# Performance work log

Measured on AMD Instinct MI355X. Metric: run time of the kernel, lower is better.

## Reference

```python
import jax, jax.numpy as jnp
import numpy as np

TOP_K = 2  # matches init_kwargs top_k


def setup_inputs() -> dict:
    key = jax.random.key(0)
    ks = jax.random.split(key, 7)
    d_model, d_ff, E = 512, 2048, 8
    B, S = 2, 2048
    std = 0.02
    return {
        "x": jax.random.normal(ks[0], (B, S, d_model), dtype=jnp.float32),
        "Wr": jax.random.normal(ks[1], (E, d_model), dtype=jnp.float32) * std,
        "br": jnp.zeros((E,), dtype=jnp.float32),
        "W1": jax.random.normal(ks[2], (E, d_model, d_ff), dtype=jnp.float32) * (1.0 / np.sqrt(d_model)),
        "b1": jnp.zeros((E, d_ff), dtype=jnp.float32),
        "W2": jax.random.normal(ks[3], (E, d_ff, d_model), dtype=jnp.float32) * (1.0 / np.sqrt(d_ff)),
        "b2": jnp.zeros((E, d_model), dtype=jnp.float32),
    }


def _moe_forward(x, Wr, br, W1, b1, W2, b2):
    leading = x.shape[:-1]
    d = x.shape[-1]
    E = Wr.shape[0]
    xf = x.reshape(-1, d)                                   # [N, d]
    N = xf.shape[0]

    # --- token router (linear head) ---
    logits = xf @ Wr.T + br                                  # [N, E]
    routing = jax.nn.softmax(logits, axis=-1)                # [N, E]
    sel_w, sel_idx = jax.lax.top_k(routing, TOP_K)           # [N, K]
    sel_w = sel_w / jnp.sum(sel_w, axis=-1, keepdims=True)   # renormalize top-k

    # combine weights as dense [N, E] (zero for unselected experts)
    combine = jnp.zeros((N, E), dtype=xf.dtype).at[
        jnp.arange(N)[:, None], sel_idx
    ].add(sel_w)                                             # [N, E]

    # --- expert FFNs (dense all-expert compute, masked combine) ---
    h = jax.nn.gelu(jnp.einsum("nd,edf->enf", xf, W1) + b1[:, None, :])  # [E, N, ff]
    y = jnp.einsum("enf,efd->end", h, W2) + b2[:, None, :]               # [E, N, d]

    out = jnp.einsum("ne,end->nd", combine, y)               # [N, d]
    return out.reshape(*leading, d)


def reference(x, Wr, br, W1, b1, W2, b2):
    return _moe_forward(x, Wr, br, W1, b1, W2, b2)
```

## Files before the change

kernel.cpp:

```cpp
#include <hip/hip_runtime.h>
#include <hip/hip_bf16.h>
#include <cstdint>

typedef unsigned short u16;
typedef __bf16 bf16_t;
typedef __bf16 bf16x8 __attribute__((ext_vector_type(8)));
typedef float f32x4 __attribute__((ext_vector_type(4)));

#define DM   512
#define DFF  2048
#define NEXP 8

__device__ __forceinline__ u16 f2bf(float f) {
  bf16_t b = (bf16_t)f;
  return __builtin_bit_cast(u16, b);
}
__device__ __forceinline__ uint32_t pack_bf2(float lo, float hi) {
  return (uint32_t)f2bf(lo) | ((uint32_t)f2bf(hi) << 16);
}
__device__ __forceinline__ float gelu_tanh(float x) {
  float x3 = x * x * x;
  float z = 0.7978845608028654f * (x + 0.044715f * x3);
  float az = fabsf(z);
  float e = __expf(2.0f * az);
  float t = 1.0f - 2.0f / (e + 1.0f);
  t = copysignf(t, z);
  return 0.5f * x * (1.0f + t);
}
__device__ __forceinline__ void async16(const u16* g, u16* l) {
  __builtin_amdgcn_global_load_lds((const __attribute__((address_space(1))) void*)g,
                                   (__attribute__((address_space(3))) void*)l, 16, 0, 0);
}

__global__ void k_transpose_cvt(const float* __restrict__ src, u16* __restrict__ dst,
                                int R, int C) {
  __shared__ u16 tile[64][65];
  int e = blockIdx.y;
  int tilesC = C >> 6;
  int bR = (blockIdx.x / tilesC) << 6;
  int bC = (blockIdx.x % tilesC) << 6;
  const float* s = src + (size_t)e * R * C;
  u16* d = dst + (size_t)e * R * C;
  int lr = threadIdx.x >> 6;
  int lc = threadIdx.x & 63;
#pragma unroll
  for (int i = 0; i < 16; ++i) {
    int r = (i << 2) + lr;
    tile[r][lc] = f2bf(s[(size_t)(bR + r) * C + bC + lc]);
  }
  __syncthreads();
#pragma unroll
  for (int i = 0; i < 16; ++i) {
    int c = (i << 2) + lr;
    d[(size_t)(bC + c) * R + bR + lc] = tile[lc][c];
  }
}

__global__ void k_router(const float* __restrict__ x, const float* __restrict__ Wr,
                         const float* __restrict__ br, int* __restrict__ sel_idx,
                         float* __restrict__ sel_w, int Ntok) {
  int wid = threadIdx.x >> 6;
  int lane = threadIdx.x & 63;
  int tok = (blockIdx.x << 2) + wid;
  if (tok >= Ntok) return;
  const float4* xr = (const float4*)(x + (size_t)tok * DM);
  float4 x0 = xr[lane * 2], x1 = xr[lane * 2 + 1];
  float logit[NEXP];
#pragma unroll
  for (int e = 0; e < NEXP; ++e) {
    const float4* wr = (const float4*)(Wr + e * DM);
    float4 w0 = wr[lane * 2], w1 = wr[lane * 2 + 1];
    float p = x0.x * w0.x + x0.y * w0.y + x0.z * w0.z + x0.w * w0.w
            + x1.x * w1.x + x1.y * w1.y + x1.z * w1.z + x1.w * w1.w;
#pragma unroll
    for (int off = 32; off; off >>= 1) p += __shfl_xor(p, off, 64);
    logit[e] = p + br[e];
  }
  if (lane == 0) {
    float mx = logit[0];
#pragma unroll
    for (int e = 1; e < NEXP; ++e) mx = fmaxf(mx, logit[e]);
    float pr[NEXP];
#pragma unroll
    for (int e = 0; e < NEXP; ++e) pr[e] = __expf(logit[e] - mx);
    int i0 = 0;
#pragma unroll
    for (int e = 1; e < NEXP; ++e) if (pr[e] > pr[i0]) i0 = e;
    int i1 = -1;
#pragma unroll
    for (int e = 0; e < NEXP; ++e) {
      if (e == i0) continue;
      if (i1 < 0 || pr[e] > pr[i1]) i1 = e;
    }
    float s2 = pr[i0] + pr[i1];
    sel_idx[tok * 2]     = i0;
    sel_idx[tok * 2 + 1] = i1;
    sel_w[tok * 2]       = pr[i0] / s2;
    sel_w[tok * 2 + 1]   = pr[i1] / s2;
  }
}

__global__ void k_scatter(const int* __restrict__ sel_idx, const float* __restrict__ sel_w,
                          int npairs, int* __restrict__ row_token, float* __restrict__ row_w,
                          int* __restrict__ pos_of, int* __restrict__ tileMeta,
                          int* __restrict__ gMeta) {
  __shared__ int cnt[NEXP], offs[NEXP], cur[NEXP];
  int tid = threadIdx.x;
  if (tid < NEXP) cnt[tid] = 0;
  __syncthreads();
  for (int p = tid; p < npairs; p += blockDim.x) atomicAdd(&cnt[sel_idx[p]], 1);
  __syncthreads();
  if (tid == 0) {
    int o = 0, nmt = 0;
    for (int e = 0; e < NEXP; ++e) {
      offs[e] = o;
      int c = cnt[e];
      int nt = (c + 127) >> 7;
      for (int t = 0; t < nt; ++t) {
        tileMeta[nmt * 3 + 0] = o + t * 128;
        tileMeta[nmt * 3 + 1] = o + c;
        tileMeta[nmt * 3 + 2] = e;
        ++nmt;
      }
      o += c;
    }
    gMeta[0] = nmt;
  }
  if (tid < NEXP) cur[tid] = 0;
  __syncthreads();
  for (int p = tid; p < npairs; p += blockDim.x) {
    int e = sel_idx[p];
    int pos = offs[e] + atomicAdd(&cur[e], 1);
    row_token[pos] = p >> 1;
    row_w[pos] = sel_w[p];
    pos_of[p] = pos;
  }
}

__global__ void k_gather(const float* __restrict__ x, const int* __restrict__ row_token,
                         u16* __restrict__ Xg, int npairs) {
  int pos = (blockIdx.x << 2) + (threadIdx.x >> 6);
  int lane = threadIdx.x & 63;
  if (pos >= npairs) return;
  int tok = row_token[pos];
  const float4* src = (const float4*)(x + (size_t)tok * DM);
  float4 a = src[lane * 2], b = src[lane * 2 + 1];
  uint4 o;
  o.x = pack_bf2(a.x, a.y);
  o.y = pack_bf2(a.z, a.w);
  o.z = pack_bf2(b.x, b.y);
  o.w = pack_bf2(b.z, b.w);
  ((uint4*)(Xg + (size_t)pos * DM))[lane] = o;
}

template <int NFULL, int K, bool GELU, bool SCALE, bool OUTBF16>
__launch_bounds__(256)
__global__ void k_gemm(const u16* __restrict__ A, const u16* __restrict__ BT,
                       const float* __restrict__ bias, const float* __restrict__ row_w,
                       void* __restrict__ Out, const int* __restrict__ tileMeta,
                       const int* __restrict__ gMeta) {
  int mt = blockIdx.x;
  if (mt >= gMeta[0]) return;
  int nt = blockIdx.y;
  int posStart = tileMeta[mt * 3 + 0];
  int segEnd   = tileMeta[mt * 3 + 1];
  int e        = tileMeta[mt * 3 + 2];

  __shared__ u16 As[128 * 64];
  __shared__ u16 Bs[128 * 64];

  int tid = threadIdx.x;
  int lane = tid & 63, wid = tid >> 6;
  int wm = wid >> 1, wn = wid & 1;

  const u16* Bex = BT + ((size_t)e * NFULL + (size_t)nt * 128) * K;

  int sRow = (wid << 3) + (lane >> 3);
  int chunkDst = lane & 7;
  const u16* aSrc[4];
  const u16* bSrc[4];
#pragma unroll
  for (int i = 0; i < 4; ++i) {
    int r = (i << 5) + sRow;
    int gra = posStart + r;
    if (gra >= segEnd) gra = segEnd - 1;
    int cs = chunkDst ^ (r & 7);
    aSrc[i] = A + (size_t)gra * K + cs * 8;
    bSrc[i] = Bex + (size_t)r * K + cs * 8;
  }

  f32x4 acc[4][4] = {};
  const char* AsB = (const char*)As;
  const char* BsB = (const char*)Bs;

  for (int kt = 0; kt < K / 64; ++kt) {
    __syncthreads();
#pragma unroll
    for (int i = 0; i < 4; ++i) {
      async16(aSrc[i] + kt * 64, As + (i << 11) + (wid << 9));
      async16(bSrc[i] + kt * 64, Bs + (i << 11) + (wid << 9));
    }
    __syncthreads();
#pragma unroll
    for (int ks = 0; ks < 2; ++ks) {
      int kByte = (ks << 6) + ((lane >> 4) << 4);
      bf16x8 av[4], bv[4];
#pragma unroll
      for (int mi = 0; mi < 4; ++mi) {
        int row = (wm << 6) + (mi << 4) + (lane & 15);
        av[mi] = *(const bf16x8*)(AsB + row * 128 + (kByte ^ ((row & 7) << 4)));
      }
#pragma unroll
      for (int ni = 0; ni < 4; ++ni) {
        int row = (wn << 6) + (ni << 4) + (lane & 15);
        bv[ni] = *(const bf16x8*)(BsB + row * 128 + (kByte ^ ((row & 7) << 4)));
      }
#pragma unroll
      for (int mi = 0; mi < 4; ++mi)
#pragma unroll
        for (int ni = 0; ni < 4; ++ni)
          acc[mi][ni] = __builtin_amdgcn_mfma_f32_16x16x32_bf16(av[mi], bv[ni], acc[mi][ni], 0, 0, 0);
    }
  }

  int laneCol = lane & 15;
  int laneRow4 = (lane >> 4) << 2;
  const float* biasE = bias + (size_t)e * NFULL;
#pragma unroll
  for (int mi = 0; mi < 4; ++mi) {
#pragma unroll
    for (int j = 0; j < 4; ++j) {
      int m = posStart + (wm << 6) + (mi << 4) + laneRow4 + j;
      if (m < segEnd) {
        float w = 1.0f;
        if constexpr (SCALE) w = row_w[m];
#pragma unroll
        for (int ni = 0; ni < 4; ++ni) {
          int n = (nt << 7) + (wn << 6) + (ni << 4) + laneCol;
          float v = acc[mi][ni][j] + biasE[n];
          if constexpr (GELU) v = gelu_tanh(v);
          if constexpr (SCALE) v *= w;
          if constexpr (OUTBF16)
            ((u16*)Out)[(size_t)m * NFULL + n] = f2bf(v);
          else
            ((float*)Out)[(size_t)m * NFULL + n] = v;
        }
      }
    }
  }
}

__global__ void k_combine(const float* __restrict__ Ys, const int* __restrict__ pos_of,
                          float* __restrict__ out, int Ntok) {
  int tok = (blockIdx.x << 1) + (threadIdx.x >> 7);
  int t = threadIdx.x & 127;
  if (tok >= Ntok) return;
  int p0 = pos_of[tok * 2], p1 = pos_of[tok * 2 + 1];
  const float4* y0 = (const float4*)(Ys + (size_t)p0 * DM);
  const float4* y1 = (const float4*)(Ys + (size_t)p1 * DM);
  float4* o = (float4*)(out + (size_t)tok * DM);
  float4 a = y0[t], b = y1[t];
  o[t] = make_float4(a.x + b.x, a.y + b.y, a.z + b.z, a.w + b.w);
}

extern "C" void kernel_launch(void* const* d_in, const int* in_sizes, int n_in,
                              void* d_out, int out_size, void* d_ws, size_t ws_size,
                              hipStream_t stream) {
  const float* x  = (const float*)d_in[0];
  const float* Wr = (const float*)d_in[1];
  const float* br = (const float*)d_in[2];
  const float* W1 = (const float*)d_in[3];
  const float* b1 = (const float*)d_in[4];
  const float* W2 = (const float*)d_in[5];
  const float* b2 = (const float*)d_in[6];
  float* out = (float*)d_out;

  int Ntok = in_sizes[0] / DM;
  int npairs = Ntok * 2;
  int maxmt = npairs / 128 + NEXP;

  char* p = (char*)d_ws;
  u16* W1T = (u16*)p;  p += (size_t)NEXP * DFF * DM * 2;
  u16* W2T = (u16*)p;  p += (size_t)NEXP * DM * DFF * 2;
  u16* Xg  = (u16*)p;  p += (size_t)npairs * DM * 2;
  u16* H   = (u16*)p;  p += (size_t)npairs * DFF * 2;
  float* Ys = (float*)p; p += (size_t)npairs * DM * 4;
  int* sel_idx   = (int*)p;   p += (size_t)npairs * 4;
  float* sel_w   = (float*)p; p += (size_t)npairs * 4;
  int* pos_of    = (int*)p;   p += (size_t)npairs * 4;
  int* row_token = (int*)p;   p += (size_t)npairs * 4;
  float* row_w   = (float*)p; p += (size_t)npairs * 4;
  int* tileMeta  = (int*)p;   p += (size_t)(maxmt * 3 + 16) * 4;
  int* gMeta     = (int*)p;   p += 64;

  k_transpose_cvt<<<dim3((DM / 64) * (DFF / 64), NEXP), 256, 0, stream>>>(W1, W1T, DM, DFF);
  k_transpose_cvt<<<dim3((DFF / 64) * (DM / 64), NEXP), 256, 0, stream>>>(W2, W2T, DFF, DM);
  k_router<<<dim3((Ntok + 3) / 4), 256, 0, stream>>>(x, Wr, br, sel_idx, sel_w, Ntok);
  k_scatter<<<dim3(1), 1024, 0, stream>>>(sel_idx, sel_w, npairs, row_token, row_w,
                                          pos_of, tileMeta, gMeta);
  k_gather<<<dim3(npairs / 4), 256, 0, stream>>>(x, row_token, Xg, npairs);
  k_gemm<DFF, DM, true, false, true>
      <<<dim3(maxmt, DFF / 128), 256, 0, stream>>>(Xg, W1T, b1, nullptr, H, tileMeta, gMeta);
  k_gemm<DM, DFF, false, true, false>
      <<<dim3(maxmt, DM / 128), 256, 0, stream>>>(H, W2T, b2, row_w, Ys, tileMeta, gMeta);
  k_combine<<<dim3(Ntok / 2), 256, 0, stream>>>(Ys, pos_of, out, Ntok);
}
```

Measured before the change: 145.8 us.

## Double-buffer GEMM loads, stage bf16 epilogue via LDS, vectorize transpose and scatter

The GEMM now double-buffers its LDS tiles so the next K-slice loads while MFMAs run, with one barrier per iteration. Its epilogue writes bf16 results into shared memory and then stores coalesced 16-byte rows. The second GEMM's intermediate output moves from fp32 to bf16, which halves the traffic for it and for the combine kernel at some cost in precision. The weight transpose uses float4 loads and packed 32-bit stores, and the scatter replaces per-element LDS atomics with wave-level ballot aggregation.

```diff
diff --git a/kernel.cpp b/kernel.cpp
--- a/kernel.cpp
+++ b/kernel.cpp
@@ -34,25 +34,30 @@
 
 __global__ void k_transpose_cvt(const float* __restrict__ src, u16* __restrict__ dst,
                                 int R, int C) {
-  __shared__ u16 tile[64][65];
+  __shared__ u16 tile[64][66];
   int e = blockIdx.y;
   int tilesC = C >> 6;
   int bR = (blockIdx.x / tilesC) << 6;
   int bC = (blockIdx.x % tilesC) << 6;
   const float* s = src + (size_t)e * R * C;
   u16* d = dst + (size_t)e * R * C;
-  int lr = threadIdx.x >> 6;
-  int lc = threadIdx.x & 63;
-#pragma unroll
-  for (int i = 0; i < 16; ++i) {
-    int r = (i << 2) + lr;
-    tile[r][lc] = f2bf(s[(size_t)(bR + r) * C + bC + lc]);
-  }
-  __syncthreads();
-#pragma unroll
-  for (int i = 0; i < 16; ++i) {
-    int c = (i << 2) + lr;
-    d[(size_t)(bC + c) * R + bR + lc] = tile[lc][c];
+  int rr = threadIdx.x >> 4;
+  int cc = (threadIdx.x & 15) << 2;
+#pragma unroll
+  for (int i = 0; i < 4; ++i) {
+    int r = (i << 4) + rr;
+    float4 v = *(const float4*)(s + (size_t)(bR + r) * C + bC + cc);
+    *(uint32_t*)&tile[r][cc]     = pack_bf2(v.x, v.y);
+    *(uint32_t*)&tile[r][cc + 2] = pack_bf2(v.z, v.w);
+  }
+  __syncthreads();
+  int c0 = threadIdx.x >> 5;
+  int j  = (threadIdx.x & 31) << 1;
+#pragma unroll
+  for (int i = 0; i < 8; ++i) {
+    int c = (i << 3) + c0;
+    uint32_t v = (uint32_t)tile[j][c] | ((uint32_t)tile[j + 1][c] << 16);
+    *(uint32_t*)(&d[(size_t)(bC + c) * R + bR + j]) = v;
   }
 }
 
@@ -106,9 +111,17 @@
                           int* __restrict__ gMeta) {
   __shared__ int cnt[NEXP], offs[NEXP], cur[NEXP];
   int tid = threadIdx.x;
-  if (tid < NEXP) cnt[tid] = 0;
-  __syncthreads();
-  for (int p = tid; p < npairs; p += blockDim.x) atomicAdd(&cnt[sel_idx[p]], 1);
+  int lane = tid & 63;
+  if (tid < NEXP) { cnt[tid] = 0; cur[tid] = 0; }
+  __syncthreads();
+  for (int p = tid; p < npairs; p += blockDim.x) {
+    int e = sel_idx[p];
+#pragma unroll
+    for (int ex = 0; ex < NEXP; ++ex) {
+      unsigned long long m = __ballot(e == ex);
+      if (lane == 0 && m) atomicAdd(&cnt[ex], __popcll(m));
+    }
+  }
   __syncthreads();
   if (tid == 0) {
     int o = 0, nmt = 0;
@@ -126,11 +139,22 @@
     }
     gMeta[0] = nmt;
   }
-  if (tid < NEXP) cur[tid] = 0;
   __syncthreads();
   for (int p = tid; p < npairs; p += blockDim.x) {
     int e = sel_idx[p];
-    int pos = offs[e] + atomicAdd(&cur[e], 1);
+    int pos = 0;
+#pragma unroll
+    for (int ex = 0; ex < NEXP; ++ex) {
+      unsigned long long m = __ballot(e == ex);
+      if (m) {
+        int leader = __ffsll((long long)m) - 1;
+        int base = 0;
+        if (lane == leader) base = atomicAdd(&cur[ex], __popcll(m));
+        base = __shfl(base, leader, 64);
+        if (e == ex)
+          pos = offs[ex] + base + __popcll(m & ((1ull << lane) - 1ull));
+      }
+    }
     row_token[pos] = p >> 1;
     row_w[pos] = sel_w[p];
     pos_of[p] = pos;
@@ -153,11 +177,11 @@
   ((uint4*)(Xg + (size_t)pos * DM))[lane] = o;
 }
 
-template <int NFULL, int K, bool GELU, bool SCALE, bool OUTBF16>
+template <int NFULL, int K, bool GELU, bool SCALE>
 __launch_bounds__(256)
 __global__ void k_gemm(const u16* __restrict__ A, const u16* __restrict__ BT,
                        const float* __restrict__ bias, const float* __restrict__ row_w,
-                       void* __restrict__ Out, const int* __restrict__ tileMeta,
+                       u16* __restrict__ Out, const int* __restrict__ tileMeta,
                        const int* __restrict__ gMeta) {
   int mt = blockIdx.x;
   if (mt >= gMeta[0]) return;
@@ -166,8 +190,7 @@
   int segEnd   = tileMeta[mt * 3 + 1];
   int e        = tileMeta[mt * 3 + 2];
 
-  __shared__ u16 As[128 * 64];
-  __shared__ u16 Bs[128 * 64];
+  __shared__ u16 smem[32768];
 
   int tid = threadIdx.x;
   int lane = tid & 63, wid = tid >> 6;
@@ -189,18 +212,27 @@
     bSrc[i] = Bex + (size_t)r * K + cs * 8;
   }
 
+  auto stage = [&](int kt, int buf) {
+    u16* as = smem + (buf << 14);
+    u16* bs = as + 8192;
+#pragma unroll
+    for (int i = 0; i < 4; ++i) {
+      async16(aSrc[i] + kt * 64, as + (i << 11) + (wid << 9));
+      async16(bSrc[i] + kt * 64, bs + (i << 11) + (wid << 9));
+    }
+  };
+
   f32x4 acc[4][4] = {};
-  const char* AsB = (const char*)As;
-  const char* BsB = (const char*)Bs;
-
-  for (int kt = 0; kt < K / 64; ++kt) {
-    __syncthreads();
-#pragma unroll
-    for (int i = 0; i < 4; ++i) {
-      async16(aSrc[i] + kt * 64, As + (i << 11) + (wid << 9));
-      async16(bSrc[i] + kt * 64, Bs + (i << 11) + (wid << 9));
-    }
-    __syncthreads();
+  constexpr int NK = K / 64;
+
+  stage(0, 0);
+  __syncthreads();
+
+  for (int kt = 0; kt < NK; ++kt) {
+    int cur = kt & 1;
+    if (kt + 1 < NK) stage(kt + 1, cur ^ 1);
+    const char* AsB = (const char*)(smem + (cur << 14));
+    const char* BsB = AsB + 16384;
 #pragma unroll
     for (int ks = 0; ks < 2; ++ks) {
       int kByte = (ks << 6) + ((lane >> 4) << 4);
@@ -221,8 +253,10 @@
         for (int ni = 0; ni < 4; ++ni)
           acc[mi][ni] = __builtin_amdgcn_mfma_f32_16x16x32_bf16(av[mi], bv[ni], acc[mi][ni], 0, 0, 0);
     }
-  }
-
+    __syncthreads();
+  }
+
+  u16* Cs = smem;
   int laneCol = lane & 15;
   int laneRow4 = (lane >> 4) << 2;
   const float* biasE = bias + (size_t)e * NFULL;
@@ -230,37 +264,54 @@
   for (int mi = 0; mi < 4; ++mi) {
 #pragma unroll
     for (int j = 0; j < 4; ++j) {
-      int m = posStart + (wm << 6) + (mi << 4) + laneRow4 + j;
-      if (m < segEnd) {
-        float w = 1.0f;
-        if constexpr (SCALE) w = row_w[m];
-#pragma unroll
-        for (int ni = 0; ni < 4; ++ni) {
-          int n = (nt << 7) + (wn << 6) + (ni << 4) + laneCol;
-          float v = acc[mi][ni][j] + biasE[n];
-          if constexpr (GELU) v = gelu_tanh(v);
-          if constexpr (SCALE) v *= w;
-          if constexpr (OUTBF16)
-            ((u16*)Out)[(size_t)m * NFULL + n] = f2bf(v);
-          else
-            ((float*)Out)[(size_t)m * NFULL + n] = v;
-        }
-      }
-    }
-  }
-}
-
-__global__ void k_combine(const float* __restrict__ Ys, const int* __restrict__ pos_of,
+      int r = (wm << 6) + (mi << 4) + laneRow4 + j;
+      int m = posStart + r;
+      float w = 1.0f;
+      if constexpr (SCALE) w = row_w[m < segEnd ? m : posStart];
+#pragma unroll
+      for (int ni = 0; ni < 4; ++ni) {
+        int cl = (wn << 6) + (ni << 4) + laneCol;
+        float v = acc[mi][ni][j] + biasE[(nt << 7) + cl];
+        if constexpr (GELU) v = gelu_tanh(v);
+        if constexpr (SCALE) v *= w;
+        Cs[r * 132 + cl] = f2bf(v);
+      }
+    }
+  }
+  __syncthreads();
+  int r0 = tid >> 4;
+  int q  = tid & 15;
+  uint4* outBase = (uint4*)(Out + (size_t)posStart * NFULL + (nt << 7));
+#pragma unroll
+  for (int i = 0; i < 8; ++i) {
+    int r = (i << 4) + r0;
+    if (posStart + r < segEnd)
+      *((uint4*)(Out + (size_t)(posStart + r) * NFULL + (nt << 7)) + q) =
+          ((uint4*)(Cs + r * 132))[q];
+  }
+  (void)outBase;
+}
+
+__global__ void k_combine(const u16* __restrict__ Ys, const int* __restrict__ pos_of,
                           float* __restrict__ out, int Ntok) {
-  int tok = (blockIdx.x << 1) + (threadIdx.x >> 7);
-  int t = threadIdx.x & 127;
+  int tok = (blockIdx.x << 2) + (threadIdx.x >> 6);
+  int lane = threadIdx.x & 63;
   if (tok >= Ntok) return;
   int p0 = pos_of[tok * 2], p1 = pos_of[tok * 2 + 1];
-  const float4* y0 = (const float4*)(Ys + (size_t)p0 * DM);
-  const float4* y1 = (const float4*)(Ys + (size_t)p1 * DM);
-  float4* o = (float4*)(out + (size_t)tok * DM);
-  float4 a = y0[t], b = y1[t];
-  o[t] = make_float4(a.x + b.x, a.y + b.y, a.z + b.z, a.w + b.w);
+  bf16x8 a = ((const bf16x8*)(Ys + (size_t)p0 * DM))[lane];
+  bf16x8 b = ((const bf16x8*)(Ys + (size_t)p1 * DM))[lane];
+  float4 o0, o1;
+  o0.x = (float)a[0] + (float)b[0];
+  o0.y = (float)a[1] + (float)b[1];
+  o0.z = (float)a[2] + (float)b[2];
+  o0.w = (float)a[3] + (float)b[3];
+  o1.x = (float)a[4] + (float)b[4];
+  o1.y = (float)a[5] + (float)b[5];
+  o1.z = (float)a[6] + (float)b[6];
+  o1.w = (float)a[7] + (float)b[7];
+  float4* o = (float4*)(out + (size_t)tok * DM + lane * 8);
+  o[0] = o0;
+  o[1] = o1;
 }
 
 extern "C" void kernel_launch(void* const* d_in, const int* in_sizes, int n_in,
@@ -284,7 +335,7 @@
   u16* W2T = (u16*)p;  p += (size_t)NEXP * DM * DFF * 2;
   u16* Xg  = (u16*)p;  p += (size_t)npairs * DM * 2;
   u16* H   = (u16*)p;  p += (size_t)npairs * DFF * 2;
-  float* Ys = (float*)p; p += (size_t)npairs * DM * 4;
+  u16* Ys  = (u16*)p;  p += (size_t)npairs * DM * 2;
   int* sel_idx   = (int*)p;   p += (size_t)npairs * 4;
   float* sel_w   = (float*)p; p += (size_t)npairs * 4;
   int* pos_of    = (int*)p;   p += (size_t)npairs * 4;
@@ -299,9 +350,9 @@
   k_scatter<<<dim3(1), 1024, 0, stream>>>(sel_idx, sel_w, npairs, row_token, row_w,
                                           pos_of, tileMeta, gMeta);
   k_gather<<<dim3(npairs / 4), 256, 0, stream>>>(x, row_token, Xg, npairs);
-  k_gemm<DFF, DM, true, false, true>
+  k_gemm<DFF, DM, true, false>
       <<<dim3(maxmt, DFF / 128), 256, 0, stream>>>(Xg, W1T, b1, nullptr, H, tileMeta, gMeta);
-  k_gemm<DM, DFF, false, true, false>
+  k_gemm<DM, DFF, false, true>
       <<<dim3(maxmt, DM / 128), 256, 0, stream>>>(H, W2T, b2, row_w, Ys, tileMeta, gMeta);
-  k_combine<<<dim3(Ntok / 2), 256, 0, stream>>>(Ys, pos_of, out, Ntok);
-}
+  k_combine<<<dim3(Ntok / 4), 256, 0, stream>>>(Ys, pos_of, out, Ntok);
+}
```

After: 156.1 us. 1.07x slower.
